# Kernel tuning notes

Hardware: AMD Instinct MI355X
Metric: run time of the kernel (lower is better)

Reference implementation:

```python
import jax, jax.numpy as jnp
import numpy as np

B = 4096
D = 1024
WEIGHT = 1.0
EPS = 1e-7  # Keras K.epsilon()


def setup_inputs() -> dict:
    key = jax.random.key(0)
    k1, k2 = jax.random.split(key)
    return {
        "left": jax.random.normal(k1, (B, D), dtype=jnp.float32),
        "right": jax.random.normal(k2, (B, D), dtype=jnp.float32),
        "temperature": jnp.zeros((1,), dtype=jnp.float32),
    }


def _l2_normalize(x):
    # matches l2_norm: sqrt(max(sum(x^2), eps))
    sq = jnp.sum(jnp.square(x), axis=-1, keepdims=True)
    return x / jnp.sqrt(jnp.maximum(sq, EPS))


def reference(left, right, temperature):
    ln = _l2_normalize(left)   # [B, D]
    rn = _l2_normalize(right)  # [B, D]
    scale = jnp.exp(temperature)  # (1,) broadcasts
    logits_left = jnp.einsum("bd,cd->bc", ln, rn) * scale   # [B, B]
    logits_right = logits_left.T                             # rn @ ln.T * scale
    prob_left = jax.nn.softmax(logits_left, axis=-1)
    prob_right = jax.nn.softmax(logits_right, axis=-1)
    # NOTE: the original calls CCE(prob, labels), i.e. y_true=prob, y_pred=eye.
    # Keras clips y_pred to [eps, 1-eps]; loss = -sum(y_true * log(clip(y_pred))).
    labels = jnp.eye(B, dtype=jnp.float32)
    log_clipped = jnp.log(jnp.clip(labels, EPS, 1.0 - EPS))  # diag: log(1-eps), off: log(eps)
    loss_left = -jnp.sum(prob_left * log_clipped)
    loss_right = -jnp.sum(prob_right * log_clipped)
    loss = (loss_left + loss_right) / 2.0 / B
    return WEIGHT * loss
```

## Files before the change

### kernel.cpp

```cpp
#include <hip/hip_runtime.h>
#include <hip/hip_bf16.h>

#define Bn 4096
#define Dk 1024
#define EPSF 1e-7f

typedef float f32x4 __attribute__((ext_vector_type(4)));

__device__ __forceinline__ void async_copy16(const void* g, void* l) {
    __builtin_amdgcn_global_load_lds((__attribute__((address_space(1))) void*)(uintptr_t)g,
                                     (__attribute__((address_space(3))) void*)l, 16, 0, 0);
}

__global__ __launch_bounds__(256)
void nrm_kernel(const float4* __restrict__ left, const float4* __restrict__ right,
                unsigned* __restrict__ lnb8, unsigned* __restrict__ rnb8,
                float* __restrict__ diag, float* __restrict__ rowsum,
                float* __restrict__ colsum)
{
    const int row = blockIdx.x;
    const int t = threadIdx.x;
    const int idx = row * (Dk / 4) + t;
    const float4 l = left[idx];
    const float4 r = right[idx];
    float sl = l.x * l.x + l.y * l.y + l.z * l.z + l.w * l.w;
    float sr = r.x * r.x + r.y * r.y + r.z * r.z + r.w * r.w;
    float slr = l.x * r.x + l.y * r.y + l.z * r.z + l.w * r.w;
    #pragma unroll
    for (int off = 1; off < 64; off <<= 1) {
        sl += __shfl_xor(sl, off);
        sr += __shfl_xor(sr, off);
        slr += __shfl_xor(slr, off);
    }
    __shared__ float red[3][4];
    const int wave = t >> 6, lane = t & 63;
    if (lane == 0) { red[0][wave] = sl; red[1][wave] = sr; red[2][wave] = slr; }
    __syncthreads();
    sl = red[0][0] + red[0][1] + red[0][2] + red[0][3];
    sr = red[1][0] + red[1][1] + red[1][2] + red[1][3];
    const float invl = 1.0f / sqrtf(fmaxf(sl, EPSF));
    const float invr = 1.0f / sqrtf(fmaxf(sr, EPSF));
    const float sL = 8.0f * invl;
    const float sR = 8.0f * invr;
    int pkL = __builtin_amdgcn_cvt_pk_fp8_f32(l.x * sL, l.y * sL, 0, false);
    pkL = __builtin_amdgcn_cvt_pk_fp8_f32(l.z * sL, l.w * sL, pkL, true);
    int pkR = __builtin_amdgcn_cvt_pk_fp8_f32(r.x * sR, r.y * sR, 0, false);
    pkR = __builtin_amdgcn_cvt_pk_fp8_f32(r.z * sR, r.w * sR, pkR, true);
    lnb8[idx] = (unsigned)pkL;
    rnb8[idx] = (unsigned)pkR;
    if (t == 0) {
        const float d = red[2][0] + red[2][1] + red[2][2] + red[2][3];
        diag[row] = d * invl * invr;
        rowsum[row] = 0.f;
        colsum[row] = 0.f;
    }
}

__global__ __launch_bounds__(256, 2)
void gemm_sm_kernel(const unsigned char* __restrict__ lnb8,
                    const unsigned char* __restrict__ rnb8,
                    const float* __restrict__ temp,
                    float* __restrict__ rowsum, float* __restrict__ colsum)
{
    __shared__ __align__(16) unsigned char As[2][128 * 64];
    __shared__ __align__(16) unsigned char Bs[2][128 * 64];

    const int tid = threadIdx.x;
    const int wave = tid >> 6;
    const int lane = tid & 63;
    const int bm0 = blockIdx.y * 128;
    const int bn0 = blockIdx.x * 128;

    const int srow = lane >> 2;
    const int sj = lane & 3;
    int goff[2];
    int lofs[2];
    #pragma unroll
    for (int i = 0; i < 2; ++i) {
        const int rloc = wave * 32 + i * 16 + srow;
        goff[i] = rloc * Dk + 16 * (sj ^ ((rloc >> 1) & 3));
        lofs[i] = (wave * 32 + i * 16) * 64;
    }
    const unsigned char* baseA = lnb8 + (size_t)bm0 * Dk;
    const unsigned char* baseB = rnb8 + (size_t)bn0 * Dk;

    const int wm = (wave & 1) * 64;
    const int wn = (wave >> 1) * 64;
    const int quad = lane >> 4;
    const int r16 = lane & 15;
    const int key = r16 & 6;
    int aoff[4], boff[4];
    #pragma unroll
    for (int i = 0; i < 4; ++i) {
        aoff[i] = (wm + i * 16 + r16) * 64 + 8 * (quad ^ key);
        boff[i] = (wn + i * 16 + r16) * 64 + 8 * (quad ^ key);
    }
    const int ks1d = 8 * ((4 + quad) ^ key) - 8 * (quad ^ key);

    f32x4 acc[4][4];
    #pragma unroll
    for (int i = 0; i < 4; ++i)
        #pragma unroll
        for (int j = 0; j < 4; ++j)
            acc[i][j] = (f32x4){0.f, 0.f, 0.f, 0.f};

    #pragma unroll
    for (int i = 0; i < 2; ++i) {
        async_copy16(baseA + goff[i], &As[0][lofs[i]]);
        async_copy16(baseB + goff[i], &Bs[0][lofs[i]]);
    }

    #pragma unroll 2
    for (int it = 0; it < 16; ++it) {
        const int cur = it & 1;
        const int nxt = cur ^ 1;
        const int knext = ((it + 1) & 15) * 64;
        #pragma unroll
        for (int i = 0; i < 2; ++i) {
            async_copy16(baseA + goff[i] + knext, &As[nxt][lofs[i]]);
            async_copy16(baseB + goff[i] + knext, &Bs[nxt][lofs[i]]);
        }
        asm volatile("s_waitcnt vmcnt(4)\n\ts_barrier" ::: "memory");
        #pragma unroll
        for (int ks = 0; ks < 2; ++ks) {
            const int d = ks ? ks1d : 0;
            long af[4], bf[4];
            #pragma unroll
            for (int i = 0; i < 4; ++i) af[i] = *(const long*)(&As[cur][aoff[i] + d]);
            #pragma unroll
            for (int i = 0; i < 4; ++i) bf[i] = *(const long*)(&Bs[cur][boff[i] + d]);
            #pragma unroll
            for (int mi = 0; mi < 4; ++mi)
                #pragma unroll
                for (int ni = 0; ni < 4; ++ni)
                    acc[mi][ni] = __builtin_amdgcn_mfma_f32_16x16x32_fp8_fp8(
                        af[mi], bf[ni], acc[mi][ni], 0, 0, 0);
        }
        asm volatile("s_barrier" ::: "memory");
    }

    const float scale = __expf(temp[0]);
    const float dq = 0.015625f * scale;
    #pragma unroll
    for (int mi = 0; mi < 4; ++mi)
        #pragma unroll
        for (int ni = 0; ni < 4; ++ni)
            #pragma unroll
            for (int r = 0; r < 4; ++r)
                acc[mi][ni][r] = __expf(dq * acc[mi][ni][r] - scale);

    #pragma unroll
    for (int mi = 0; mi < 4; ++mi) {
        #pragma unroll
        for (int r = 0; r < 4; ++r) {
            float v = acc[mi][0][r] + acc[mi][1][r] + acc[mi][2][r] + acc[mi][3][r];
            v += __shfl_xor(v, 1);
            v += __shfl_xor(v, 2);
            v += __shfl_xor(v, 4);
            v += __shfl_xor(v, 8);
            if (r16 == 0)
                atomicAdd(&rowsum[bm0 + wm + mi * 16 + quad * 4 + r], v);
        }
    }
    #pragma unroll
    for (int ni = 0; ni < 4; ++ni) {
        float v = 0.f;
        #pragma unroll
        for (int mi = 0; mi < 4; ++mi)
            #pragma unroll
            for (int r = 0; r < 4; ++r)
                v += acc[mi][ni][r];
        v += __shfl_xor(v, 16);
        v += __shfl_xor(v, 32);
        if (quad == 0)
            atomicAdd(&colsum[bn0 + wn + ni * 16 + r16], v);
    }
}

__global__ __launch_bounds__(256)
void loss_kernel(const float* __restrict__ diag, const float* __restrict__ rowsum,
                 const float* __restrict__ colsum, const float* __restrict__ temp,
                 float* __restrict__ out)
{
    const int t = threadIdx.x;
    const float scale = __expf(temp[0]);
    float dL = 0.f, dR = 0.f;
    for (int i = t; i < Bn; i += 256) {
        const float e = __expf(scale * (diag[i] - 1.0f));
        dL += e * __builtin_amdgcn_rcpf(rowsum[i]);
        dR += e * __builtin_amdgcn_rcpf(colsum[i]);
    }
    #pragma unroll
    for (int off = 1; off < 64; off <<= 1) {
        dL += __shfl_xor(dL, off);
        dR += __shfl_xor(dR, off);
    }
    __shared__ float rd[2][4];
    const int wave = t >> 6, lane = t & 63;
    if (lane == 0) { rd[0][wave] = dL; rd[1][wave] = dR; }
    __syncthreads();
    if (t == 0) {
        dL = rd[0][0] + rd[0][1] + rd[0][2] + rd[0][3];
        dR = rd[1][0] + rd[1][1] + rd[1][2] + rd[1][3];
        const float logeps = logf(EPSF);
        const float log1m = logf(1.0f - EPSF);
        const float lossL = -(dL * log1m + ((float)Bn - dL) * logeps);
        const float lossR = -(dR * log1m + ((float)Bn - dR) * logeps);
        out[0] = (lossL + lossR) * 0.5f / (float)Bn;
    }
}

extern "C" void kernel_launch(void* const* d_in, const int* in_sizes, int n_in,
                              void* d_out, int out_size, void* d_ws, size_t ws_size,
                              hipStream_t stream) {
    (void)in_sizes; (void)n_in; (void)out_size; (void)ws_size;
    const float* left = (const float*)d_in[0];
    const float* right = (const float*)d_in[1];
    const float* temp = (const float*)d_in[2];

    char* ws = (char*)d_ws;
    unsigned char* lnb8 = (unsigned char*)ws;
    unsigned char* rnb8 = (unsigned char*)(ws + (size_t)Bn * Dk);
    float* diag = (float*)(ws + 2 * (size_t)Bn * Dk);
    float* rowsum = diag + Bn;
    float* colsum = rowsum + Bn;

    nrm_kernel<<<Bn, 256, 0, stream>>>((const float4*)left, (const float4*)right,
                                       (unsigned*)lnb8, (unsigned*)rnb8, diag, rowsum, colsum);
    dim3 g2(Bn / 128, Bn / 128);
    gemm_sm_kernel<<<g2, 256, 0, stream>>>(lnb8, rnb8, temp, rowsum, colsum);
    loss_kernel<<<1, 256, 0, stream>>>(diag, rowsum, colsum, temp, (float*)d_out);
}
```

Before: 119.1 us.

## Give each wave private LDS tiles to remove block-wide barriers in GEMM

Each wave now stages its own 64-row slices of the fp8 A and B operands into a private LDS region. The per-iteration s_barrier calls are replaced with per-wave vmcnt/lgkmcnt waits, so waves no longer synchronise with each other during the K loop. The aim is to cut barrier stalls and let waves run independently. In exchange, LDS use per block doubles, and A/B rows shared by waves are fetched redundantly from L2/global memory.

```diff
diff --git a/kernel.cpp b/kernel.cpp
--- a/kernel.cpp
+++ b/kernel.cpp
@@ -62,8 +62,8 @@
                     const float* __restrict__ temp,
                     float* __restrict__ rowsum, float* __restrict__ colsum)
 {
-    __shared__ __align__(16) unsigned char As[2][128 * 64];
-    __shared__ __align__(16) unsigned char Bs[2][128 * 64];
+    __shared__ __align__(16) unsigned char SA[2][4][4096];
+    __shared__ __align__(16) unsigned char SB[2][4][4096];
 
     const int tid = threadIdx.x;
     const int wave = tid >> 6;
@@ -71,30 +71,23 @@
     const int bm0 = blockIdx.y * 128;
     const int bn0 = blockIdx.x * 128;
 
+    const int wm = (wave & 1) * 64;
+    const int wn = (wave >> 1) * 64;
+
     const int srow = lane >> 2;
     const int sj = lane & 3;
-    int goff[2];
-    int lofs[2];
-    #pragma unroll
-    for (int i = 0; i < 2; ++i) {
-        const int rloc = wave * 32 + i * 16 + srow;
-        goff[i] = rloc * Dk + 16 * (sj ^ ((rloc >> 1) & 3));
-        lofs[i] = (wave * 32 + i * 16) * 64;
-    }
-    const unsigned char* baseA = lnb8 + (size_t)bm0 * Dk;
-    const unsigned char* baseB = rnb8 + (size_t)bn0 * Dk;
-
-    const int wm = (wave & 1) * 64;
-    const int wn = (wave >> 1) * 64;
+    const int gcol = 16 * (sj ^ ((srow >> 1) & 3));
+    const unsigned char* baseA = lnb8 + (size_t)(bm0 + wm) * Dk;
+    const unsigned char* baseB = rnb8 + (size_t)(bn0 + wn) * Dk;
+    const int goff = srow * Dk + gcol;
+
     const int quad = lane >> 4;
     const int r16 = lane & 15;
     const int key = r16 & 6;
-    int aoff[4], boff[4];
-    #pragma unroll
-    for (int i = 0; i < 4; ++i) {
-        aoff[i] = (wm + i * 16 + r16) * 64 + 8 * (quad ^ key);
-        boff[i] = (wn + i * 16 + r16) * 64 + 8 * (quad ^ key);
-    }
+    int aoff[4];
+    #pragma unroll
+    for (int i = 0; i < 4; ++i)
+        aoff[i] = (i * 16 + r16) * 64 + 8 * (quad ^ key);
     const int ks1d = 8 * ((4 + quad) ^ key) - 8 * (quad ^ key);
 
     f32x4 acc[4][4];
@@ -105,9 +98,9 @@
             acc[i][j] = (f32x4){0.f, 0.f, 0.f, 0.f};
 
     #pragma unroll
-    for (int i = 0; i < 2; ++i) {
-        async_copy16(baseA + goff[i], &As[0][lofs[i]]);
-        async_copy16(baseB + goff[i], &Bs[0][lofs[i]]);
+    for (int i = 0; i < 4; ++i) {
+        async_copy16(baseA + goff + i * 16 * Dk, &SA[0][wave][i * 1024]);
+        async_copy16(baseB + goff + i * 16 * Dk, &SB[0][wave][i * 1024]);
     }
 
     #pragma unroll 2
@@ -115,20 +108,23 @@
         const int cur = it & 1;
         const int nxt = cur ^ 1;
         const int knext = ((it + 1) & 15) * 64;
-        #pragma unroll
-        for (int i = 0; i < 2; ++i) {
-            async_copy16(baseA + goff[i] + knext, &As[nxt][lofs[i]]);
-            async_copy16(baseB + goff[i] + knext, &Bs[nxt][lofs[i]]);
+        asm volatile("s_waitcnt lgkmcnt(0)" ::: "memory");
+        #pragma unroll
+        for (int i = 0; i < 4; ++i) {
+            async_copy16(baseA + goff + i * 16 * Dk + knext, &SA[nxt][wave][i * 1024]);
+            async_copy16(baseB + goff + i * 16 * Dk + knext, &SB[nxt][wave][i * 1024]);
         }
-        asm volatile("s_waitcnt vmcnt(4)\n\ts_barrier" ::: "memory");
+        asm volatile("s_waitcnt vmcnt(8)" ::: "memory");
+        const unsigned char* As = &SA[cur][wave][0];
+        const unsigned char* Bs = &SB[cur][wave][0];
         #pragma unroll
         for (int ks = 0; ks < 2; ++ks) {
             const int d = ks ? ks1d : 0;
             long af[4], bf[4];
             #pragma unroll
-            for (int i = 0; i < 4; ++i) af[i] = *(const long*)(&As[cur][aoff[i] + d]);
-            #pragma unroll
-            for (int i = 0; i < 4; ++i) bf[i] = *(const long*)(&Bs[cur][boff[i] + d]);
+            for (int i = 0; i < 4; ++i) af[i] = *(const long*)(As + aoff[i] + d);
+            #pragma unroll
+            for (int i = 0; i < 4; ++i) bf[i] = *(const long*)(Bs + aoff[i] + d);
             #pragma unroll
             for (int mi = 0; mi < 4; ++mi)
                 #pragma unroll
@@ -136,7 +132,6 @@
                     acc[mi][ni] = __builtin_amdgcn_mfma_f32_16x16x32_fp8_fp8(
                         af[mi], bf[ni], acc[mi][ni], 0, 0, 0);
         }
-        asm volatile("s_barrier" ::: "memory");
     }
 
     const float scale = __expf(temp[0]);
```

Result: slower. 126.5 us (+6.2%).

## Permute fp8 K layout so GEMM fetches both k-steps with 16-byte LDS reads

Applied to the files above, without the earlier changes.

The normalisation kernel now writes the fp8 operands in a permuted order within each 64-byte K chunk, so that the two 8-byte fragments a lane needs for consecutive k-steps sit next to each other. The GEMM replaces two 8-byte LDS reads per fragment with one 16-byte read, changing the swizzle key to match. It also raises the launch-bounds occupancy hint from 2 to 3 blocks per CU, which may squeeze registers for the 64-float accumulator tile and risk spills.

```diff
diff --git a/kernel.cpp b/kernel.cpp
--- a/kernel.cpp
+++ b/kernel.cpp
@@ -6,6 +6,7 @@
 #define EPSF 1e-7f
 
 typedef float f32x4 __attribute__((ext_vector_type(4)));
+typedef long long2_t __attribute__((ext_vector_type(2)));
 
 __device__ __forceinline__ void async_copy16(const void* g, void* l) {
     __builtin_amdgcn_global_load_lds((__attribute__((address_space(1))) void*)(uintptr_t)g,
@@ -14,7 +15,7 @@
 
 __global__ __launch_bounds__(256)
 void nrm_kernel(const float4* __restrict__ left, const float4* __restrict__ right,
-                unsigned* __restrict__ lnb8, unsigned* __restrict__ rnb8,
+                unsigned char* __restrict__ lnb8, unsigned char* __restrict__ rnb8,
                 float* __restrict__ diag, float* __restrict__ rowsum,
                 float* __restrict__ colsum)
 {
@@ -46,8 +47,12 @@
     pkL = __builtin_amdgcn_cvt_pk_fp8_f32(l.z * sL, l.w * sL, pkL, true);
     int pkR = __builtin_amdgcn_cvt_pk_fp8_f32(r.x * sR, r.y * sR, 0, false);
     pkR = __builtin_amdgcn_cvt_pk_fp8_f32(r.z * sR, r.w * sR, pkR, true);
-    lnb8[idx] = (unsigned)pkL;
-    rnb8[idx] = (unsigned)pkR;
+    const int k0 = 4 * t;
+    const int g = k0 >> 6;
+    const int kl = k0 & 63;
+    const int dst = row * Dk + (g << 6) + (((kl & 31) >> 3) << 4) + ((kl >> 5) << 3) + (kl & 7);
+    *(unsigned*)(lnb8 + dst) = (unsigned)pkL;
+    *(unsigned*)(rnb8 + dst) = (unsigned)pkR;
     if (t == 0) {
         const float d = red[2][0] + red[2][1] + red[2][2] + red[2][3];
         diag[row] = d * invl * invr;
@@ -56,7 +61,7 @@
     }
 }
 
-__global__ __launch_bounds__(256, 2)
+__global__ __launch_bounds__(256, 3)
 void gemm_sm_kernel(const unsigned char* __restrict__ lnb8,
                     const unsigned char* __restrict__ rnb8,
                     const float* __restrict__ temp,
@@ -88,14 +93,13 @@
     const int wn = (wave >> 1) * 64;
     const int quad = lane >> 4;
     const int r16 = lane & 15;
-    const int key = r16 & 6;
+    const int skey = (r16 >> 1) & 3;
     int aoff[4], boff[4];
     #pragma unroll
     for (int i = 0; i < 4; ++i) {
-        aoff[i] = (wm + i * 16 + r16) * 64 + 8 * (quad ^ key);
-        boff[i] = (wn + i * 16 + r16) * 64 + 8 * (quad ^ key);
-    }
-    const int ks1d = 8 * ((4 + quad) ^ key) - 8 * (quad ^ key);
+        aoff[i] = (wm + i * 16 + r16) * 64 + 16 * (quad ^ skey);
+        boff[i] = (wn + i * 16 + r16) * 64 + 16 * (quad ^ skey);
+    }
 
     f32x4 acc[4][4];
     #pragma unroll
@@ -121,21 +125,23 @@
             async_copy16(baseB + goff[i] + knext, &Bs[nxt][lofs[i]]);
         }
         asm volatile("s_waitcnt vmcnt(4)\n\ts_barrier" ::: "memory");
-        #pragma unroll
-        for (int ks = 0; ks < 2; ++ks) {
-            const int d = ks ? ks1d : 0;
-            long af[4], bf[4];
-            #pragma unroll
-            for (int i = 0; i < 4; ++i) af[i] = *(const long*)(&As[cur][aoff[i] + d]);
-            #pragma unroll
-            for (int i = 0; i < 4; ++i) bf[i] = *(const long*)(&Bs[cur][boff[i] + d]);
-            #pragma unroll
-            for (int mi = 0; mi < 4; ++mi)
-                #pragma unroll
-                for (int ni = 0; ni < 4; ++ni)
-                    acc[mi][ni] = __builtin_amdgcn_mfma_f32_16x16x32_fp8_fp8(
-                        af[mi], bf[ni], acc[mi][ni], 0, 0, 0);
-        }
+        long2_t af01[4], bf01[4];
+        #pragma unroll
+        for (int i = 0; i < 4; ++i) af01[i] = *(const long2_t*)(&As[cur][aoff[i]]);
+        #pragma unroll
+        for (int i = 0; i < 4; ++i) bf01[i] = *(const long2_t*)(&Bs[cur][boff[i]]);
+        #pragma unroll
+        for (int mi = 0; mi < 4; ++mi)
+            #pragma unroll
+            for (int ni = 0; ni < 4; ++ni)
+                acc[mi][ni] = __builtin_amdgcn_mfma_f32_16x16x32_fp8_fp8(
+                    af01[mi].x, bf01[ni].x, acc[mi][ni], 0, 0, 0);
+        #pragma unroll
+        for (int mi = 0; mi < 4; ++mi)
+            #pragma unroll
+            for (int ni = 0; ni < 4; ++ni)
+                acc[mi][ni] = __builtin_amdgcn_mfma_f32_16x16x32_fp8_fp8(
+                    af01[mi].y, bf01[ni].y, acc[mi][ni], 0, 0, 0);
         asm volatile("s_barrier" ::: "memory");
     }
 
@@ -226,7 +232,7 @@
     float* colsum = rowsum + Bn;
 
     nrm_kernel<<<Bn, 256, 0, stream>>>((const float4*)left, (const float4*)right,
-                                       (unsigned*)lnb8, (unsigned*)rnb8, diag, rowsum, colsum);
+                                       lnb8, rnb8, diag, rowsum, colsum);
     dim3 g2(Bn / 128, Bn / 128);
     gemm_sm_kernel<<<g2, 256, 0, stream>>>(lnb8, rnb8, temp, rowsum, colsum);
     loss_kernel<<<1, 256, 0, stream>>>(diag, rowsum, colsum, temp, (float*)d_out);
```

After: 115.8 us. 1.03x faster.
